# Kernel tuning notes

Measured on AMD Instinct MI355X. Metric: run time of the kernel, lower is better.

The kernel has to match this reference:

```python
import jax, jax.numpy as jnp
import numpy as np

NL, NH, H, FF, V, P = 12, 12, 768, 3072, 30522, 512
B, L, S = 4, 512, 8
DH = H // NH


def _layer_norm(x, g, b, eps=1e-12):
    m = x.mean(-1, keepdims=True)
    v = jnp.mean((x - m) ** 2, axis=-1, keepdims=True)
    return (x - m) * jax.lax.rsqrt(v + eps) * g + b


def setup_inputs() -> dict:
    key = jax.random.key(0)
    ks = iter(jax.random.split(key, 40))
    pm = lambda shape: jax.random.normal(next(ks), shape, jnp.float32) * 0.02
    inp = {
        'word_emb': pm((V, H)), 'pos_emb': pm((P, H)), 'type_emb': pm((2, H)),
        'emb_ln_g': jnp.ones((H,), jnp.float32), 'emb_ln_b': jnp.zeros((H,), jnp.float32),
        'Wq': pm((NL, H, H)), 'bq': jnp.zeros((NL, H), jnp.float32),
        'Wk': pm((NL, H, H)), 'bk': jnp.zeros((NL, H), jnp.float32),
        'Wv': pm((NL, H, H)), 'bv': jnp.zeros((NL, H), jnp.float32),
        'Wo': pm((NL, H, H)), 'bo': jnp.zeros((NL, H), jnp.float32),
        'attn_ln_g': jnp.ones((NL, H), jnp.float32), 'attn_ln_b': jnp.zeros((NL, H), jnp.float32),
        'W1': pm((NL, H, FF)), 'b1': jnp.zeros((NL, FF), jnp.float32),
        'W2': pm((NL, FF, H)), 'b2': jnp.zeros((NL, H), jnp.float32),
        'ffn_ln_g': jnp.ones((NL, H), jnp.float32), 'ffn_ln_b': jnp.zeros((NL, H), jnp.float32),
        'fc_w': pm((H,)), 'fc_b': jnp.zeros((), jnp.float32),
    }
    inp['input_ids'] = jax.random.randint(next(ks), (B, L), 0, V)
    inp['token_type_ids'] = jnp.zeros((B, L), jnp.int32)
    # valid-length prefix attention_mask and sorted bos_locations (history = 64)
    vl = np.array([384 + 16 * (i % 8) for i in range(B)])
    hist = 64
    am = (np.arange(L)[None, :] < vl[:, None]).astype(np.int32)
    bos = np.stack([hist + (np.arange(S) * (v - hist)) // S for v in vl]).astype(np.int64)
    inp['attention_mask'] = jnp.asarray(am)
    inp['bos_locations'] = jnp.asarray(bos)
    return inp


def _forward(word_emb, pos_emb, type_emb, emb_ln_g, emb_ln_b,
             Wq, bq, Wk, bk, Wv, bv, Wo, bo, attn_ln_g, attn_ln_b,
             W1, b1, W2, b2, ffn_ln_g, ffn_ln_b, fc_w, fc_b,
             input_ids, token_type_ids, attention_mask, bos_locations):
    Bs, Ls = input_ids.shape
    t = jnp.arange(Ls)
    valid_len = attention_mask.sum(-1)                       # [B]
    hist = bos_locations[:, 0]                               # [B] history length
    # segment id per token: number of bos positions <= t, minus 1 (-1 in history)
    seg = (bos_locations[:, :, None] <= t[None, None, :]).sum(1) - 1   # [B,L]
    valid = t[None, :] < valid_len[:, None]                  # [B,L]
    # block-diagonal candidate attention mask (history rows/cols fully visible)
    p = t[None, :, None]
    q = t[None, None, :]
    hist_pq = (p < hist[:, None, None]) | (q < hist[:, None, None])
    same_seg = seg[:, :, None] == seg[:, None, :]
    mask = valid[:, :, None] & valid[:, None, :] & (hist_pq | same_seg)  # [B,L,L]
    bias = jnp.where(mask, 0.0, -10000.0).astype(jnp.float32)[:, None, :, :]  # [B,1,L,L]

    # BERT embeddings
    x = word_emb[input_ids] + pos_emb[t][None] + type_emb[token_type_ids]
    x = _layer_norm(x, emb_ln_g, emb_ln_b)
    scale = 1.0 / jnp.sqrt(jnp.asarray(DH, x.dtype))

    for l in range(NL):
        qh = (x @ Wq[l] + bq[l]).reshape(Bs, Ls, NH, DH)
        kh = (x @ Wk[l] + bk[l]).reshape(Bs, Ls, NH, DH)
        vh = (x @ Wv[l] + bv[l]).reshape(Bs, Ls, NH, DH)
        scores = jnp.einsum('bqhd,bkhd->bhqk', qh, kh) * scale + bias
        probs = jax.nn.softmax(scores, axis=-1)
        ctx = jnp.einsum('bhqk,bkhd->bqhd', probs, vh).reshape(Bs, Ls, H)
        x = _layer_norm(x + ctx @ Wo[l] + bo[l], attn_ln_g[l], attn_ln_b[l])
        h = jax.nn.gelu(x @ W1[l] + b1[l], approximate=False)
        x = _layer_norm(x + h @ W2[l] + b2[l], ffn_ln_g[l], ffn_ln_b[l])

    # variable-length segment mean pooling via membership matmul
    starts = bos_locations                                   # [B,S]
    ends = jnp.concatenate([bos_locations[:, 1:], valid_len[:, None]], axis=1)
    memb = ((t[None, None, :] >= starts[:, :, None]) &
            (t[None, None, :] < ends[:, :, None])).astype(x.dtype)        # [B,S,L]
    pooled = jnp.einsum('bsl,bld->bsd', memb, x) / memb.sum(-1, keepdims=True)
    logits = pooled @ fc_w + fc_b                            # [B,S]
    return jnp.squeeze(logits)


def reference(word_emb, pos_emb, type_emb, emb_ln_g, emb_ln_b,
              Wq, bq, Wk, bk, Wv, bv, Wo, bo, attn_ln_g, attn_ln_b,
              W1, b1, W2, b2, ffn_ln_g, ffn_ln_b, fc_w, fc_b,
              input_ids, token_type_ids, attention_mask, bos_locations):
    return _forward(word_emb, pos_emb, type_emb, emb_ln_g, emb_ln_b,
                    Wq, bq, Wk, bk, Wv, bv, Wo, bo, attn_ln_g, attn_ln_b,
                    W1, b1, W2, b2, ffn_ln_g, ffn_ln_b, fc_w, fc_b,
                    input_ids, token_type_ids, attention_mask, bos_locations)
```

## Files before the change

kernel.cpp:

```cpp
#include <hip/hip_runtime.h>
#include <math.h>

#define HH 768
#define FF 3072
#define NL 12
#define NH 12
#define DH 64
#define BB 4
#define LL 512
#define SS 8
#define MM (BB*LL)
#define WQSZ (HH*HH)
#define W1SZ (HH*FF)

typedef short bf16x8 __attribute__((ext_vector_type(8)));
typedef float f32x4 __attribute__((ext_vector_type(4)));

__device__ inline ushort f2b(float f) {
  unsigned u = __float_as_uint(f);
  unsigned r = (u + 0x7FFFu + ((u >> 16) & 1u)) >> 16;
  return (ushort)r;
}

__global__ void prep_kernel(const int* __restrict__ am, const int* __restrict__ bos,
                            int* __restrict__ seg, int* __restrict__ vl) {
  int b = blockIdx.x;
  int t = threadIdx.x;
  __shared__ int red[512];
  red[t] = am[b*LL + t];
  __syncthreads();
  for (int off = 256; off > 0; off >>= 1) {
    if (t < off) red[t] += red[t+off];
    __syncthreads();
  }
  if (t == 0) vl[b] = red[0];
  int cnt = 0;
  #pragma unroll
  for (int s = 0; s < SS; s++) cnt += (bos[b*SS + s] <= t) ? 1 : 0;
  seg[b*LL + t] = cnt - 1;
}

__global__ __launch_bounds__(256) void embed_ln_kernel(
    const float* __restrict__ word_emb, const float* __restrict__ pos_emb,
    const float* __restrict__ type_emb, const float* __restrict__ g,
    const float* __restrict__ bta, const int* __restrict__ ids,
    const int* __restrict__ tts, float* __restrict__ x, ushort* __restrict__ xb)
{
  int row = blockIdx.x;
  int l = row & (LL-1);
  int t = threadIdx.x;
  int id = ids[row];
  int ty = tts[row];
  float v[3];
  float s = 0.f, sq = 0.f;
  #pragma unroll
  for (int j = 0; j < 3; j++) {
    int c = t + j*256;
    float val = word_emb[(size_t)id*HH + c] + pos_emb[l*HH + c] + type_emb[ty*HH + c];
    v[j] = val; s += val; sq += val*val;
  }
  __shared__ float rs[256], rq[256];
  rs[t] = s; rq[t] = sq;
  __syncthreads();
  for (int off = 128; off > 0; off >>= 1) {
    if (t < off) { rs[t] += rs[t+off]; rq[t] += rq[t+off]; }
    __syncthreads();
  }
  float mean = rs[0] / HH;
  float var  = rq[0] / HH - mean*mean;
  float inv  = rsqrtf(var + 1e-12f);
  #pragma unroll
  for (int j = 0; j < 3; j++) {
    int c = t + j*256;
    float o = (v[j]-mean)*inv*g[c] + bta[c];
    x[(size_t)row*HH + c] = o;
    xb[(size_t)row*HH + c] = f2b(o);
  }
}

__global__ __launch_bounds__(256) void add_ln2_kernel(
    const float* __restrict__ xin, const float* __restrict__ y1,
    const float* __restrict__ y2, const float* __restrict__ g,
    const float* __restrict__ bta, float* __restrict__ xout, ushort* __restrict__ xb)
{
  int row = blockIdx.x;
  int t = threadIdx.x;
  float v[3];
  float s = 0.f, sq = 0.f;
  #pragma unroll
  for (int j = 0; j < 3; j++) {
    int c = t + j*256;
    size_t ix = (size_t)row*HH + c;
    float val = xin[ix] + y1[ix] + y2[ix];
    v[j] = val; s += val; sq += val*val;
  }
  __shared__ float rs[256], rq[256];
  rs[t] = s; rq[t] = sq;
  __syncthreads();
  for (int off = 128; off > 0; off >>= 1) {
    if (t < off) { rs[t] += rs[t+off]; rq[t] += rq[t+off]; }
    __syncthreads();
  }
  float mean = rs[0] / HH;
  float var  = rq[0] / HH - mean*mean;
  float inv  = rsqrtf(var + 1e-12f);
  #pragma unroll
  for (int j = 0; j < 3; j++) {
    int c = t + j*256;
    float o = (v[j]-mean)*inv*g[c] + bta[c];
    xout[(size_t)row*HH + c] = o;
    xb[(size_t)row*HH + c] = f2b(o);
  }
}

__global__ __launch_bounds__(256) void convw_kernel(
    const float* __restrict__ Wq, const float* __restrict__ Wk,
    const float* __restrict__ Wv, const float* __restrict__ Wo,
    const float* __restrict__ W1, const float* __restrict__ W2,
    ushort* __restrict__ wbuf)
{
  int idx = blockIdx.x;
  const float* src; ushort* dst; int Nsrc, dstK, kt, nt;
  if (idx < 576) {
    int mat = idx / 144, t = idx % 144;
    src = (mat == 0) ? Wq : (mat == 1) ? Wk : (mat == 2) ? Wv : Wo;
    dst = wbuf + (size_t)mat * WQSZ;
    Nsrc = HH; dstK = HH; kt = t % 12; nt = t / 12;
  } else if (idx < 1152) {
    int t = idx - 576;
    src = W1; dst = wbuf + (size_t)4 * WQSZ;
    Nsrc = FF; dstK = HH; kt = t % 12; nt = t / 12;
  } else {
    int t = idx - 1152;
    src = W2; dst = wbuf + (size_t)4 * WQSZ + W1SZ;
    Nsrc = HH; dstK = FF; kt = t % 48; nt = t / 48;
  }
  int k0 = kt * 64, n0 = nt * 64;
  __shared__ ushort tt[64][72];
  int tid = threadIdx.x;
  int r = tid >> 4, c = (tid & 15) << 2;
  #pragma unroll
  for (int i = 0; i < 4; i++) {
    int rr = r + i*16;
    float4 v = *(const float4*)&src[(size_t)(k0+rr)*Nsrc + n0 + c];
    tt[c+0][rr] = f2b(v.x); tt[c+1][rr] = f2b(v.y);
    tt[c+2][rr] = f2b(v.z); tt[c+3][rr] = f2b(v.w);
  }
  __syncthreads();
  #pragma unroll
  for (int it = 0; it < 2; it++) {
    int n = it*32 + (tid >> 3);
    int k = (tid & 7) << 3;
    ushort tmp8[8];
    #pragma unroll
    for (int j = 0; j < 8; j++) tmp8[j] = tt[n][k+j];
    *(uint4*)&dst[(size_t)(n0+n)*dstK + k0 + k] = *(const uint4*)tmp8;
  }
}

struct GArg { const ushort* Bt; const float* bias; float* Cf; ushort* Cb; };
struct GArg3 { GArg a[3]; };

template<int ACT, int WF32, int WBF16, int SPLITK>
__global__ __launch_bounds__(256) void gemm_mfma64(
    const ushort* __restrict__ A, GArg3 ga, int M, int N, int K)
{
  const GArg g = SPLITK ? ga.a[0] : ga.a[blockIdx.z];
  __shared__ __align__(16) ushort As[2][64*64];
  __shared__ __align__(16) ushort Bs[2][64*64];
  const int tid = threadIdx.x;
  const int lane = tid & 63, wid = tid >> 6;
  const int wm = wid >> 1, wn = wid & 1;
  const int m0 = blockIdx.y * 64, n0 = blockIdx.x * 64;
  int kbeg = 0, kend = K;
  if (SPLITK) { int kh = K >> 1; kbeg = blockIdx.z * kh; kend = kbeg + kh; }

  auto STAGE = [&](int buf, int k0) {
    #pragma unroll
    for (int j = 0; j < 2; j++) {
      int cbase = j*256 + wid*64;
      int c = cbase + lane;
      int r = c >> 3;
      int kk = ((c & 7) ^ (r & 7)) << 3;
      __builtin_amdgcn_global_load_lds(
        (const __attribute__((address_space(1))) void*)(A + (size_t)(m0+r)*K + k0 + kk),
        (__attribute__((address_space(3))) void*)(&As[buf][cbase*8]), 16, 0, 0);
    }
    #pragma unroll
    for (int j = 0; j < 2; j++) {
      int cbase = j*256 + wid*64;
      int c = cbase + lane;
      int r = c >> 3;
      int kk = ((c & 7) ^ (r & 7)) << 3;
      __builtin_amdgcn_global_load_lds(
        (const __attribute__((address_space(1))) void*)(g.Bt + (size_t)(n0+r)*K + k0 + kk),
        (__attribute__((address_space(3))) void*)(&Bs[buf][cbase*8]), 16, 0, 0);
    }
  };

  f32x4 acc[2][2] = {};
  const int NT = (kend - kbeg) >> 6;
  STAGE(0, kbeg);
  __syncthreads();
  int cur = 0;
  for (int t = 0; t < NT; ++t) {
    if (t + 1 < NT) STAGE(cur ^ 1, kbeg + (t+1)*64);
    bf16x8 af[2][2], bfv[2][2];
    #pragma unroll
    for (int mi = 0; mi < 2; mi++) {
      int row = wm*32 + mi*16 + (lane & 15);
      #pragma unroll
      for (int ks = 0; ks < 2; ks++) {
        int kb = (ks*64 + ((lane >> 4) << 4)) ^ ((row & 7) << 4);
        af[mi][ks] = *(const bf16x8*)((const char*)&As[cur][0] + row*128 + kb);
      }
    }
    #pragma unroll
    for (int ni = 0; ni < 2; ni++) {
      int row = wn*32 + ni*16 + (lane & 15);
      #pragma unroll
      for (int ks = 0; ks < 2; ks++) {
        int kb = (ks*64 + ((lane >> 4) << 4)) ^ ((row & 7) << 4);
        bfv[ni][ks] = *(const bf16x8*)((const char*)&Bs[cur][0] + row*128 + kb);
      }
    }
    #pragma unroll
    for (int ks = 0; ks < 2; ks++)
      #pragma unroll
      for (int mi = 0; mi < 2; mi++)
        #pragma unroll
        for (int ni = 0; ni < 2; ni++)
          acc[mi][ni] = __builtin_amdgcn_mfma_f32_16x16x32_bf16(af[mi][ks], bfv[ni][ks], acc[mi][ni], 0, 0, 0);
    __syncthreads();
    cur ^= 1;
  }

  #pragma unroll
  for (int mi = 0; mi < 2; mi++) {
    #pragma unroll
    for (int ni = 0; ni < 2; ni++) {
      int col = n0 + wn*32 + ni*16 + (lane & 15);
      float bv = (!SPLITK || blockIdx.z == 0) ? g.bias[col] : 0.f;
      #pragma unroll
      for (int r = 0; r < 4; r++) {
        int row = m0 + wm*32 + mi*16 + (lane >> 4)*4 + r;
        float v = acc[mi][ni][r] + bv;
        if (ACT) v = 0.5f * v * (1.0f + erff(v * 0.70710678118654752f));
        if (WF32)  g.Cf[(SPLITK ? (size_t)blockIdx.z*M*N : 0) + (size_t)row*N + col] = v;
        if (WBF16) g.Cb[(size_t)row*N + col] = f2b(v);
      }
    }
  }
}

__global__ __launch_bounds__(256) void attn_mfma_kernel(
    const ushort* __restrict__ Q, const ushort* __restrict__ Kp, const ushort* __restrict__ Vp,
    ushort* __restrict__ ctx, const int* __restrict__ seg, const int* __restrict__ vl,
    const int* __restrict__ bos)
{
  const int q0 = blockIdx.x * 64;
  const int h  = blockIdx.y;
  const int b  = blockIdx.z;
  const int tid = threadIdx.x;
  const int lane = tid & 63;
  const int wid = tid >> 6;

  __shared__ __align__(16) char Ks[8192];
  __shared__ __align__(16) char Vt[8192];
  __shared__ __align__(16) char Ps[4][2048];
  __shared__ int segk[64];

  const int qrow_frag = q0 + wid*16 + (lane & 15);
  bf16x8 qf[2];
  #pragma unroll
  for (int c = 0; c < 2; c++)
    qf[c] = *(const bf16x8*)&Q[((size_t)(b*LL + qrow_frag))*HH + h*DH + 32*c + (lane >> 4)*8];

  const int vlb  = vl[b];
  const int hist = bos[b*SS];
  int segq[4]; bool qvalid[4], qhist[4];
  #pragma unroll
  for (int r = 0; r < 4; r++) {
    int qg = q0 + wid*16 + (lane >> 4)*4 + r;
    segq[r]   = seg[b*LL + qg];
    qvalid[r] = qg < vlb;
    qhist[r]  = qg < hist;
  }

  float mrow[4], lrow[4];
  #pragma unroll
  for (int r = 0; r < 4; r++) { mrow[r] = -1e30f; lrow[r] = 0.f; }
  f32x4 Oacc[4] = {};

  for (int k0 = 0; k0 < LL; k0 += 64) {
    __syncthreads();
    #pragma unroll
    for (int p = 0; p < 2; p++) {
      int r  = (tid >> 3) + 32*p;
      int c8 = (tid & 7) * 8;
      uint4 kv = *(const uint4*)&Kp[((size_t)(b*LL + k0 + r))*HH + h*DH + c8];
      *(uint4*)(Ks + (r*128 + ((c8*2) ^ ((r & 7) << 4)))) = kv;
    }
    #pragma unroll
    for (int p = 0; p < 2; p++) {
      int k  = lane;
      int d0 = wid*8 + 32*p;
      uint4 vv = *(const uint4*)&Vp[((size_t)(b*LL + k0 + k))*HH + h*DH + d0];
      const ushort* pv = (const ushort*)&vv;
      #pragma unroll
      for (int j = 0; j < 8; j++) {
        int d = d0 + j;
        *(ushort*)(Vt + (d*128 + ((k*2) ^ ((d & 7) << 4)))) = pv[j];
      }
    }
    if (tid < 64) segk[tid] = seg[b*LL + k0 + tid];
    __syncthreads();

    f32x4 sacc[4] = {};
    #pragma unroll
    for (int t = 0; t < 4; t++) {
      int krow = (lane & 15) + 16*t;
      #pragma unroll
      for (int c = 0; c < 2; c++) {
        bf16x8 kf = *(const bf16x8*)(Ks + (krow*128 +
                      (((32*c + (lane >> 4)*8)*2) ^ ((krow & 7) << 4))));
        sacc[t] = __builtin_amdgcn_mfma_f32_16x16x32_bf16(qf[c], kf, sacc[t], 0, 0, 0);
      }
    }

    #pragma unroll
    for (int t = 0; t < 4; t++) {
      int kg = k0 + (lane & 15) + 16*t;
      bool kvalid = kg < vlb;
      bool khist  = kg < hist;
      int  sk     = segk[(lane & 15) + 16*t];
      #pragma unroll
      for (int r = 0; r < 4; r++) {
        bool ok = qvalid[r] && kvalid && (khist || qhist[r] || (segq[r] == sk));
        sacc[t][r] = sacc[t][r]*0.125f + (ok ? 0.f : -10000.f);
      }
    }

    float scl[4];
    #pragma unroll
    for (int r = 0; r < 4; r++) {
      float rm = fmaxf(fmaxf(sacc[0][r], sacc[1][r]), fmaxf(sacc[2][r], sacc[3][r]));
      rm = fmaxf(rm, __shfl_xor(rm, 1));
      rm = fmaxf(rm, __shfl_xor(rm, 2));
      rm = fmaxf(rm, __shfl_xor(rm, 4));
      rm = fmaxf(rm, __shfl_xor(rm, 8));
      float mnew = fmaxf(mrow[r], rm);
      scl[r] = __expf(mrow[r] - mnew);
      float rsum = 0.f;
      #pragma unroll
      for (int t = 0; t < 4; t++) {
        float p = __expf(sacc[t][r] - mnew);
        sacc[t][r] = p;
        rsum += p;
      }
      rsum += __shfl_xor(rsum, 1);
      rsum += __shfl_xor(rsum, 2);
      rsum += __shfl_xor(rsum, 4);
      rsum += __shfl_xor(rsum, 8);
      mrow[r] = mnew;
      lrow[r] = lrow[r]*scl[r] + rsum;
    }

    char* Pl = Ps[wid];
    #pragma unroll
    for (int t = 0; t < 4; t++) {
      #pragma unroll
      for (int r = 0; r < 4; r++) {
        int q = (lane >> 4)*4 + r;
        int k = (lane & 15) + 16*t;
        *(ushort*)(Pl + (q*128 + ((k*2) ^ ((q & 7) << 4)))) = f2b(sacc[t][r]);
      }
    }
    asm volatile("s_waitcnt lgkmcnt(0)" ::: "memory");
    bf16x8 pf[2];
    #pragma unroll
    for (int c = 0; c < 2; c++) {
      int q = lane & 15;
      int k = 32*c + (lane >> 4)*8;
      pf[c] = *(const bf16x8*)(Pl + (q*128 + ((k*2) ^ ((q & 7) << 4))));
    }

    #pragma unroll
    for (int nt = 0; nt < 4; nt++) {
      #pragma unroll
      for (int r = 0; r < 4; r++) Oacc[nt][r] *= scl[r];
      int d = (lane & 15) + 16*nt;
      #pragma unroll
      for (int c = 0; c < 2; c++) {
        int k = 32*c + (lane >> 4)*8;
        bf16x8 vf = *(const bf16x8*)(Vt + (d*128 + ((k*2) ^ ((d & 7) << 4))));
        Oacc[nt] = __builtin_amdgcn_mfma_f32_16x16x32_bf16(pf[c], vf, Oacc[nt], 0, 0, 0);
      }
    }
  }

  #pragma unroll
  for (int nt = 0; nt < 4; nt++) {
    #pragma unroll
    for (int r = 0; r < 4; r++) {
      int q = q0 + wid*16 + (lane >> 4)*4 + r;
      int d = h*DH + (lane & 15) + 16*nt;
      ctx[(size_t)(b*LL + q)*HH + d] = f2b(Oacc[nt][r] / lrow[r]);
    }
  }
}

__global__ __launch_bounds__(256) void rowdot_kernel(const float* __restrict__ x,
                                                     const float* __restrict__ w,
                                                     float* __restrict__ rd) {
  int row = blockIdx.x;
  int t = threadIdx.x;
  float s = 0.f;
  #pragma unroll
  for (int j = 0; j < 3; j++) {
    int c = t + j*256;
    s = fmaf(x[(size_t)row*HH + c], w[c], s);
  }
  __shared__ float red[256];
  red[t] = s;
  __syncthreads();
  for (int off = 128; off > 0; off >>= 1) {
    if (t < off) red[t] += red[t+off];
    __syncthreads();
  }
  if (t == 0) rd[row] = red[0];
}

__global__ void logits_kernel(const float* __restrict__ rd, const int* __restrict__ bos,
                              const int* __restrict__ vl, const float* __restrict__ fcb,
                              float* __restrict__ out) {
  int i = threadIdx.x;
  if (i >= BB*SS) return;
  int b = i / SS, s = i % SS;
  int start = bos[b*SS + s];
  int end   = (s == SS-1) ? vl[b] : bos[b*SS + s + 1];
  float sum = 0.f;
  for (int t = start; t < end; t++) sum += rd[b*LL + t];
  out[i] = sum / (float)(end - start) + fcb[0];
}

extern "C" void kernel_launch(void* const* d_in, const int* in_sizes, int n_in,
                              void* d_out, int out_size, void* d_ws, size_t ws_size,
                              hipStream_t stream) {
  const float* word_emb  = (const float*)d_in[0];
  const float* pos_emb   = (const float*)d_in[1];
  const float* type_emb  = (const float*)d_in[2];
  const float* emb_ln_g  = (const float*)d_in[3];
  const float* emb_ln_b  = (const float*)d_in[4];
  const float* Wq        = (const float*)d_in[5];
  const float* bq        = (const float*)d_in[6];
  const float* Wk        = (const float*)d_in[7];
  const float* bk        = (const float*)d_in[8];
  const float* Wv        = (const float*)d_in[9];
  const float* bv        = (const float*)d_in[10];
  const float* Wo        = (const float*)d_in[11];
  const float* bo        = (const float*)d_in[12];
  const float* attn_ln_g = (const float*)d_in[13];
  const float* attn_ln_b = (const float*)d_in[14];
  const float* W1        = (const float*)d_in[15];
  const float* b1        = (const float*)d_in[16];
  const float* W2        = (const float*)d_in[17];
  const float* b2        = (const float*)d_in[18];
  const float* ffn_ln_g  = (const float*)d_in[19];
  const float* ffn_ln_b  = (const float*)d_in[20];
  const float* fc_w      = (const float*)d_in[21];
  const float* fc_b      = (const float*)d_in[22];
  const int* input_ids   = (const int*)d_in[23];
  const int* token_type  = (const int*)d_in[24];
  const int* am          = (const int*)d_in[25];
  const int* bos         = (const int*)d_in[26];
  float* out = (float*)d_out;

  char* w = (char*)d_ws;
  float*  x       = (float*)w;  w += (size_t)MM*HH*4;
  float*  tmp     = (float*)w;  w += (size_t)2*MM*HH*4;
  ushort* qkv_bf  = (ushort*)w; w += (size_t)3*MM*HH*2;
  ushort* x_bf    = (ushort*)w; w += (size_t)MM*HH*2;
  ushort* ctx_bf  = (ushort*)w; w += (size_t)MM*HH*2;
  ushort* hbuf_bf = (ushort*)w; w += (size_t)MM*FF*2;
  ushort* wbuf    = (ushort*)w; w += (size_t)(4*WQSZ + 2*W1SZ)*2;
  float*  rd      = (float*)w;  w += (size_t)MM*4;
  int*    seg     = (int*)w;    w += (size_t)MM*4;
  int*    vl      = (int*)w;    w += 64;

  prep_kernel<<<BB, 512, 0, stream>>>(am, bos, seg, vl);
  embed_ln_kernel<<<MM, 256, 0, stream>>>(word_emb, pos_emb, type_emb,
                                          emb_ln_g, emb_ln_b, input_ids, token_type, x, x_bf);

  dim3 gqkv(HH/64, MM/64, 3);
  dim3 g_ff1(FF/64, MM/64, 1);
  dim3 g_sk(HH/64, MM/64, 2);
  dim3 gattn(LL/64, NH, BB);

  for (int l = 0; l < NL; l++) {
    convw_kernel<<<1728, 256, 0, stream>>>(Wq + (size_t)l*WQSZ, Wk + (size_t)l*WQSZ,
                                           Wv + (size_t)l*WQSZ, Wo + (size_t)l*WQSZ,
                                           W1 + (size_t)l*W1SZ, W2 + (size_t)l*W1SZ, wbuf);

    GArg3 gq;
    for (int z = 0; z < 3; z++) {
      gq.a[z].Bt   = wbuf + (size_t)z*WQSZ;
      gq.a[z].bias = (z == 0 ? bq : z == 1 ? bk : bv) + (size_t)l*HH;
      gq.a[z].Cf   = nullptr;
      gq.a[z].Cb   = qkv_bf + (size_t)z*MM*HH;
    }
    gemm_mfma64<0,0,1,0><<<gqkv, 256, 0, stream>>>(x_bf, gq, MM, HH, HH);

    attn_mfma_kernel<<<gattn, 256, 0, stream>>>(qkv_bf, qkv_bf + (size_t)MM*HH,
                                                qkv_bf + (size_t)2*MM*HH, ctx_bf, seg, vl, bos);

    GArg3 go = {};
    go.a[0].Bt = wbuf + (size_t)3*WQSZ; go.a[0].bias = bo + (size_t)l*HH;
    go.a[0].Cf = tmp; go.a[0].Cb = nullptr;
    gemm_mfma64<0,1,0,1><<<g_sk, 256, 0, stream>>>(ctx_bf, go, MM, HH, HH);

    add_ln2_kernel<<<MM, 256, 0, stream>>>(x, tmp, tmp + (size_t)MM*HH,
                                           attn_ln_g + (size_t)l*HH,
                                           attn_ln_b + (size_t)l*HH, x, x_bf);

    GArg3 g1 = {};
    g1.a[0].Bt = wbuf + (size_t)4*WQSZ; g1.a[0].bias = b1 + (size_t)l*FF;
    g1.a[0].Cf = nullptr; g1.a[0].Cb = hbuf_bf;
    gemm_mfma64<1,0,1,0><<<g_ff1, 256, 0, stream>>>(x_bf, g1, MM, FF, HH);

    GArg3 g2 = {};
    g2.a[0].Bt = wbuf + (size_t)4*WQSZ + W1SZ; g2.a[0].bias = b2 + (size_t)l*HH;
    g2.a[0].Cf = tmp; g2.a[0].Cb = nullptr;
    gemm_mfma64<0,1,0,1><<<g_sk, 256, 0, stream>>>(hbuf_bf, g2, MM, HH, FF);

    add_ln2_kernel<<<MM, 256, 0, stream>>>(x, tmp, tmp + (size_t)MM*HH,
                                           ffn_ln_g + (size_t)l*HH,
                                           ffn_ln_b + (size_t)l*HH, x, x_bf);
  }

  rowdot_kernel<<<MM, 256, 0, stream>>>(x, fc_w, rd);
  logits_kernel<<<1, 64, 0, stream>>>(rd, bos, vl, fc_b, out);
}
```

Before: 1.456 ms.

## Convert all layer weights in one launch and retile GEMMs to 128x64 with K=32

All twelve layers' weights are converted to transposed bf16 in a single up-front kernel into a per-layer buffer, replacing the per-layer conversion launch. The GEMM kernel is retiled to 128x64 output tiles with a K step of 32 and a 4-way XOR swizzle. QKV is computed as one GEMM over a concatenated N=2304 weight matrix, with the epilogue scattering columns to separate Q, K and V buffers. This trades a larger workspace and fewer blocks for better per-block reuse and fewer launches.

```diff
diff --git a/kernel.cpp b/kernel.cpp
--- a/kernel.cpp
+++ b/kernel.cpp
@@ -12,6 +12,10 @@
 #define MM (BB*LL)
 #define WQSZ (HH*HH)
 #define W1SZ (HH*FF)
+#define LWB 7077888
+#define OFF_WO 1769472
+#define OFF_W1 2359296
+#define OFF_W2 4718592
 
 typedef short bf16x8 __attribute__((ext_vector_type(8)));
 typedef float f32x4 __attribute__((ext_vector_type(4)));
@@ -113,36 +117,46 @@
   }
 }
 
-__global__ __launch_bounds__(256) void convw_kernel(
+__global__ __launch_bounds__(256) void convw_all_kernel(
     const float* __restrict__ Wq, const float* __restrict__ Wk,
     const float* __restrict__ Wv, const float* __restrict__ Wo,
     const float* __restrict__ W1, const float* __restrict__ W2,
     ushort* __restrict__ wbuf)
 {
   int idx = blockIdx.x;
-  const float* src; ushort* dst; int Nsrc, dstK, kt, nt;
-  if (idx < 576) {
-    int mat = idx / 144, t = idx % 144;
-    src = (mat == 0) ? Wq : (mat == 1) ? Wk : (mat == 2) ? Wv : Wo;
-    dst = wbuf + (size_t)mat * WQSZ;
-    Nsrc = HH; dstK = HH; kt = t % 12; nt = t / 12;
-  } else if (idx < 1152) {
-    int t = idx - 576;
-    src = W1; dst = wbuf + (size_t)4 * WQSZ;
-    Nsrc = FF; dstK = HH; kt = t % 12; nt = t / 12;
+  int l = idx / 1728;
+  int t0 = idx % 1728;
+  size_t base = (size_t)l * LWB;
+  const float* src; ushort* dst; int Nsrc, dstK, k0, n0src, n0dst;
+  if (t0 < 432) {
+    int nt = t0 / 12, kt = t0 % 12;
+    int z = nt / 12, ntl = nt % 12;
+    src = (z == 0 ? Wq : z == 1 ? Wk : Wv) + (size_t)l*WQSZ;
+    dst = wbuf + base;
+    Nsrc = HH; dstK = HH; k0 = kt*64; n0src = ntl*64; n0dst = nt*64;
+  } else if (t0 < 576) {
+    int t = t0 - 432; int nt = t / 12, kt = t % 12;
+    src = Wo + (size_t)l*WQSZ;
+    dst = wbuf + base + OFF_WO;
+    Nsrc = HH; dstK = HH; k0 = kt*64; n0src = n0dst = nt*64;
+  } else if (t0 < 1152) {
+    int t = t0 - 576; int nt = t / 12, kt = t % 12;
+    src = W1 + (size_t)l*W1SZ;
+    dst = wbuf + base + OFF_W1;
+    Nsrc = FF; dstK = HH; k0 = kt*64; n0src = n0dst = nt*64;
   } else {
-    int t = idx - 1152;
-    src = W2; dst = wbuf + (size_t)4 * WQSZ + W1SZ;
-    Nsrc = HH; dstK = FF; kt = t % 48; nt = t / 48;
-  }
-  int k0 = kt * 64, n0 = nt * 64;
+    int t = t0 - 1152; int nt = t / 48, kt = t % 48;
+    src = W2 + (size_t)l*W1SZ;
+    dst = wbuf + base + OFF_W2;
+    Nsrc = HH; dstK = FF; k0 = kt*64; n0src = n0dst = nt*64;
+  }
   __shared__ ushort tt[64][72];
   int tid = threadIdx.x;
   int r = tid >> 4, c = (tid & 15) << 2;
   #pragma unroll
   for (int i = 0; i < 4; i++) {
     int rr = r + i*16;
-    float4 v = *(const float4*)&src[(size_t)(k0+rr)*Nsrc + n0 + c];
+    float4 v = *(const float4*)&src[(size_t)(k0+rr)*Nsrc + n0src + c];
     tt[c+0][rr] = f2b(v.x); tt[c+1][rr] = f2b(v.y);
     tt[c+2][rr] = f2b(v.z); tt[c+3][rr] = f2b(v.w);
   }
@@ -154,100 +168,104 @@
     ushort tmp8[8];
     #pragma unroll
     for (int j = 0; j < 8; j++) tmp8[j] = tt[n][k+j];
-    *(uint4*)&dst[(size_t)(n0+n)*dstK + k0 + k] = *(const uint4*)tmp8;
-  }
-}
-
-struct GArg { const ushort* Bt; const float* bias; float* Cf; ushort* Cb; };
-struct GArg3 { GArg a[3]; };
-
-template<int ACT, int WF32, int WBF16, int SPLITK>
-__global__ __launch_bounds__(256) void gemm_mfma64(
-    const ushort* __restrict__ A, GArg3 ga, int M, int N, int K)
+    *(uint4*)&dst[(size_t)(n0dst+n)*dstK + k0 + k] = *(const uint4*)tmp8;
+  }
+}
+
+template<int MODE>
+__global__ __launch_bounds__(256) void gemm_bt(
+    const ushort* __restrict__ A, const ushort* __restrict__ Bt,
+    const float* __restrict__ ba, const float* __restrict__ bb,
+    const float* __restrict__ bc, float* __restrict__ Cf,
+    ushort* __restrict__ Cb, int M, int N, int K)
 {
-  const GArg g = SPLITK ? ga.a[0] : ga.a[blockIdx.z];
-  __shared__ __align__(16) ushort As[2][64*64];
-  __shared__ __align__(16) ushort Bs[2][64*64];
+  __shared__ __align__(16) ushort As[2][128*32];
+  __shared__ __align__(16) ushort Bs[2][64*32];
   const int tid = threadIdx.x;
   const int lane = tid & 63, wid = tid >> 6;
   const int wm = wid >> 1, wn = wid & 1;
-  const int m0 = blockIdx.y * 64, n0 = blockIdx.x * 64;
-  int kbeg = 0, kend = K;
-  if (SPLITK) { int kh = K >> 1; kbeg = blockIdx.z * kh; kend = kbeg + kh; }
+  const int m0 = blockIdx.y * 128, n0 = blockIdx.x * 64;
+  int kbeg = 0, NT = K >> 5;
+  if (MODE == 2) { int kh = K >> 1; kbeg = blockIdx.z * kh; NT = kh >> 5; }
 
   auto STAGE = [&](int buf, int k0) {
     #pragma unroll
     for (int j = 0; j < 2; j++) {
-      int cbase = j*256 + wid*64;
-      int c = cbase + lane;
-      int r = c >> 3;
-      int kk = ((c & 7) ^ (r & 7)) << 3;
+      int c = j*256 + tid;
+      int r = c >> 2;
+      int kk = ((c & 3) ^ (r & 3)) << 3;
       __builtin_amdgcn_global_load_lds(
         (const __attribute__((address_space(1))) void*)(A + (size_t)(m0+r)*K + k0 + kk),
-        (__attribute__((address_space(3))) void*)(&As[buf][cbase*8]), 16, 0, 0);
-    }
-    #pragma unroll
-    for (int j = 0; j < 2; j++) {
-      int cbase = j*256 + wid*64;
-      int c = cbase + lane;
-      int r = c >> 3;
-      int kk = ((c & 7) ^ (r & 7)) << 3;
+        (__attribute__((address_space(3))) void*)(&As[buf][c*8]), 16, 0, 0);
+    }
+    {
+      int c = tid;
+      int r = c >> 2;
+      int kk = ((c & 3) ^ (r & 3)) << 3;
       __builtin_amdgcn_global_load_lds(
-        (const __attribute__((address_space(1))) void*)(g.Bt + (size_t)(n0+r)*K + k0 + kk),
-        (__attribute__((address_space(3))) void*)(&Bs[buf][cbase*8]), 16, 0, 0);
+        (const __attribute__((address_space(1))) void*)(Bt + (size_t)(n0+r)*K + k0 + kk),
+        (__attribute__((address_space(3))) void*)(&Bs[buf][c*8]), 16, 0, 0);
     }
   };
 
-  f32x4 acc[2][2] = {};
-  const int NT = (kend - kbeg) >> 6;
+  f32x4 acc[4][2] = {};
   STAGE(0, kbeg);
   __syncthreads();
   int cur = 0;
   for (int t = 0; t < NT; ++t) {
-    if (t + 1 < NT) STAGE(cur ^ 1, kbeg + (t+1)*64);
-    bf16x8 af[2][2], bfv[2][2];
-    #pragma unroll
-    for (int mi = 0; mi < 2; mi++) {
-      int row = wm*32 + mi*16 + (lane & 15);
-      #pragma unroll
-      for (int ks = 0; ks < 2; ks++) {
-        int kb = (ks*64 + ((lane >> 4) << 4)) ^ ((row & 7) << 4);
-        af[mi][ks] = *(const bf16x8*)((const char*)&As[cur][0] + row*128 + kb);
-      }
+    if (t + 1 < NT) STAGE(cur ^ 1, kbeg + (t+1)*32);
+    bf16x8 af[4], bf[2];
+    #pragma unroll
+    for (int mi = 0; mi < 4; mi++) {
+      int r = wm*64 + mi*16 + (lane & 15);
+      int slot = (lane >> 4) ^ (r & 3);
+      af[mi] = *(const bf16x8*)(&As[cur][r*32 + slot*8]);
     }
     #pragma unroll
     for (int ni = 0; ni < 2; ni++) {
-      int row = wn*32 + ni*16 + (lane & 15);
-      #pragma unroll
-      for (int ks = 0; ks < 2; ks++) {
-        int kb = (ks*64 + ((lane >> 4) << 4)) ^ ((row & 7) << 4);
-        bfv[ni][ks] = *(const bf16x8*)((const char*)&Bs[cur][0] + row*128 + kb);
-      }
-    }
-    #pragma unroll
-    for (int ks = 0; ks < 2; ks++)
-      #pragma unroll
-      for (int mi = 0; mi < 2; mi++)
-        #pragma unroll
-        for (int ni = 0; ni < 2; ni++)
-          acc[mi][ni] = __builtin_amdgcn_mfma_f32_16x16x32_bf16(af[mi][ks], bfv[ni][ks], acc[mi][ni], 0, 0, 0);
+      int r = wn*32 + ni*16 + (lane & 15);
+      int slot = (lane >> 4) ^ (r & 3);
+      bf[ni] = *(const bf16x8*)(&Bs[cur][r*32 + slot*8]);
+    }
+    #pragma unroll
+    for (int mi = 0; mi < 4; mi++)
+      #pragma unroll
+      for (int ni = 0; ni < 2; ni++)
+        acc[mi][ni] = __builtin_amdgcn_mfma_f32_16x16x32_bf16(af[mi], bf[ni], acc[mi][ni], 0, 0, 0);
     __syncthreads();
     cur ^= 1;
   }
 
   #pragma unroll
-  for (int mi = 0; mi < 2; mi++) {
+  for (int mi = 0; mi < 4; mi++) {
     #pragma unroll
     for (int ni = 0; ni < 2; ni++) {
       int col = n0 + wn*32 + ni*16 + (lane & 15);
-      float bv = (!SPLITK || blockIdx.z == 0) ? g.bias[col] : 0.f;
-      #pragma unroll
-      for (int r = 0; r < 4; r++) {
-        int row = m0 + wm*32 + mi*16 + (lane >> 4)*4 + r;
-        float v = acc[mi][ni][r] + bv;
-        if (ACT) v = 0.5f * v * (1.0f + erff(v * 0.70710678118654752f));
-        if (WF32)  g.Cf[(SPLITK ? (size_t)blockIdx.z*M*N : 0) + (size_t)row*N + col] = v;
-        if (WBF16) g.Cb[(size_t)row*N + col] = f2b(v);
+      if (MODE == 0) {
+        int z = (col >= 1536) ? 2 : (col >= 768 ? 1 : 0);
+        int cc = col - z*768;
+        float bvv = (z == 0 ? ba : z == 1 ? bb : bc)[cc];
+        #pragma unroll
+        for (int r = 0; r < 4; r++) {
+          int row = m0 + wm*64 + mi*16 + (lane >> 4)*4 + r;
+          Cb[(size_t)z*MM*HH + (size_t)row*HH + cc] = f2b(acc[mi][ni][r] + bvv);
+        }
+      } else if (MODE == 1) {
+        float bvv = ba[col];
+        #pragma unroll
+        for (int r = 0; r < 4; r++) {
+          int row = m0 + wm*64 + mi*16 + (lane >> 4)*4 + r;
+          float v = acc[mi][ni][r] + bvv;
+          v = 0.5f * v * (1.0f + erff(v * 0.70710678118654752f));
+          Cb[(size_t)row*N + col] = f2b(v);
+        }
+      } else {
+        float bvv = (blockIdx.z == 0) ? ba[col] : 0.f;
+        #pragma unroll
+        for (int r = 0; r < 4; r++) {
+          int row = m0 + wm*64 + mi*16 + (lane >> 4)*4 + r;
+          Cf[(size_t)blockIdx.z*M*N + (size_t)row*N + col] = acc[mi][ni][r] + bvv;
+        }
       }
     }
   }
@@ -483,55 +501,46 @@
   ushort* x_bf    = (ushort*)w; w += (size_t)MM*HH*2;
   ushort* ctx_bf  = (ushort*)w; w += (size_t)MM*HH*2;
   ushort* hbuf_bf = (ushort*)w; w += (size_t)MM*FF*2;
-  ushort* wbuf    = (ushort*)w; w += (size_t)(4*WQSZ + 2*W1SZ)*2;
+  ushort* wbuf    = (ushort*)w; w += (size_t)NL*LWB*2;
   float*  rd      = (float*)w;  w += (size_t)MM*4;
   int*    seg     = (int*)w;    w += (size_t)MM*4;
   int*    vl      = (int*)w;    w += 64;
 
   prep_kernel<<<BB, 512, 0, stream>>>(am, bos, seg, vl);
+  convw_all_kernel<<<NL*1728, 256, 0, stream>>>(Wq, Wk, Wv, Wo, W1, W2, wbuf);
   embed_ln_kernel<<<MM, 256, 0, stream>>>(word_emb, pos_emb, type_emb,
                                           emb_ln_g, emb_ln_b, input_ids, token_type, x, x_bf);
 
-  dim3 gqkv(HH/64, MM/64, 3);
-  dim3 g_ff1(FF/64, MM/64, 1);
-  dim3 g_sk(HH/64, MM/64, 2);
+  dim3 gqkv(2304/64, MM/128);
+  dim3 g_ff1(FF/64, MM/128);
+  dim3 g_sk(HH/64, MM/128, 2);
   dim3 gattn(LL/64, NH, BB);
 
   for (int l = 0; l < NL; l++) {
-    convw_kernel<<<1728, 256, 0, stream>>>(Wq + (size_t)l*WQSZ, Wk + (size_t)l*WQSZ,
-                                           Wv + (size_t)l*WQSZ, Wo + (size_t)l*WQSZ,
-                                           W1 + (size_t)l*W1SZ, W2 + (size_t)l*W1SZ, wbuf);
-
-    GArg3 gq;
-    for (int z = 0; z < 3; z++) {
-      gq.a[z].Bt   = wbuf + (size_t)z*WQSZ;
-      gq.a[z].bias = (z == 0 ? bq : z == 1 ? bk : bv) + (size_t)l*HH;
-      gq.a[z].Cf   = nullptr;
-      gq.a[z].Cb   = qkv_bf + (size_t)z*MM*HH;
-    }
-    gemm_mfma64<0,0,1,0><<<gqkv, 256, 0, stream>>>(x_bf, gq, MM, HH, HH);
+    const ushort* Wqkv_t = wbuf + (size_t)l*LWB;
+    const ushort* Wo_t   = wbuf + (size_t)l*LWB + OFF_WO;
+    const ushort* W1_t   = wbuf + (size_t)l*LWB + OFF_W1;
+    const ushort* W2_t   = wbuf + (size_t)l*LWB + OFF_W2;
+
+    gemm_bt<0><<<gqkv, 256, 0, stream>>>(x_bf, Wqkv_t,
+        bq + (size_t)l*HH, bk + (size_t)l*HH, bv + (size_t)l*HH,
+        nullptr, qkv_bf, MM, 2304, HH);
 
     attn_mfma_kernel<<<gattn, 256, 0, stream>>>(qkv_bf, qkv_bf + (size_t)MM*HH,
                                                 qkv_bf + (size_t)2*MM*HH, ctx_bf, seg, vl, bos);
 
-    GArg3 go = {};
-    go.a[0].Bt = wbuf + (size_t)3*WQSZ; go.a[0].bias = bo + (size_t)l*HH;
-    go.a[0].Cf = tmp; go.a[0].Cb = nullptr;
-    gemm_mfma64<0,1,0,1><<<g_sk, 256, 0, stream>>>(ctx_bf, go, MM, HH, HH);
+    gemm_bt<2><<<g_sk, 256, 0, stream>>>(ctx_bf, Wo_t,
+        bo + (size_t)l*HH, nullptr, nullptr, tmp, nullptr, MM, HH, HH);
 
     add_ln2_kernel<<<MM, 256, 0, stream>>>(x, tmp, tmp + (size_t)MM*HH,
                                            attn_ln_g + (size_t)l*HH,
                                            attn_ln_b + (size_t)l*HH, x, x_bf);
 
-    GArg3 g1 = {};
-    g1.a[0].Bt = wbuf + (size_t)4*WQSZ; g1.a[0].bias = b1 + (size_t)l*FF;
-    g1.a[0].Cf = nullptr; g1.a[0].Cb = hbuf_bf;
-    gemm_mfma64<1,0,1,0><<<g_ff1, 256, 0, stream>>>(x_bf, g1, MM, FF, HH);
-
-    GArg3 g2 = {};
-    g2.a[0].Bt = wbuf + (size_t)4*WQSZ + W1SZ; g2.a[0].bias = b2 + (size_t)l*HH;
-    g2.a[0].Cf = tmp; g2.a[0].Cb = nullptr;
-    gemm_mfma64<0,1,0,1><<<g_sk, 256, 0, stream>>>(hbuf_bf, g2, MM, HH, FF);
+    gemm_bt<1><<<g_ff1, 256, 0, stream>>>(x_bf, W1_t,
+        b1 + (size_t)l*FF, nullptr, nullptr, nullptr, hbuf_bf, MM, FF, HH);
+
+    gemm_bt<2><<<g_sk, 256, 0, stream>>>(hbuf_bf, W2_t,
+        b2 + (size_t)l*HH, nullptr, nullptr, tmp, nullptr, MM, HH, FF);
 
     add_ln2_kernel<<<MM, 256, 0, stream>>>(x, tmp, tmp + (size_t)MM*HH,
                                            ffn_ln_g + (size_t)l*HH,
```

New measurement: 1.645 ms. 13.0% more time.
